# Kernel tuning notes

Hardware: AMD Instinct MI355X
Metric: run time of the kernel (lower is better)

Reference implementation:

```python
import jax, jax.numpy as jnp
import numpy as np

N = 200000          # nodes
E = 800000          # edges (avg degree ~4, molecular graphs)
F_IN = 128          # dataset.num_node_features
HID = 32            # hidden_channels -> widths 32, 64, 128
N_TASKS = 128       # dataset.num_tasks
G = 8000            # number of graphs in the batch
EPS = 1e-5


def _glorot(key, shape):
    fan_in, fan_out = shape[0], shape[1]
    lim = np.sqrt(6.0 / (fan_in + fan_out)).astype(np.float32)
    return jax.random.uniform(key, shape, jnp.float32, -lim, lim)


def setup_inputs() -> dict:
    key = jax.random.key(0)
    ks = jax.random.split(key, 16)
    x = jax.random.normal(ks[0], (N, F_IN), jnp.float32)
    edge_index = jax.random.randint(ks[1], (2, E), 0, N, jnp.int64)
    batch = jnp.sort(jax.random.randint(ks[2], (N,), 0, G, jnp.int64))
    return {
        "x": x,
        "edge_index": edge_index,
        "batch": batch,
        "norm_w": jnp.ones((1,), jnp.float32),
        "norm_b": jnp.zeros((1,), jnp.float32),
        "W1": _glorot(ks[3], (F_IN, HID)),
        "b1": jnp.zeros((HID,), jnp.float32),
        "W2": _glorot(ks[4], (HID, 2 * HID)),
        "b2": jnp.zeros((2 * HID,), jnp.float32),
        "W3": _glorot(ks[5], (2 * HID, 4 * HID)),
        "b3": jnp.zeros((4 * HID,), jnp.float32),
        "lin1_W": _glorot(ks[6], (4 * HID, 256)),
        "lin1_b": jnp.zeros((256,), jnp.float32),
        "lin2_W": _glorot(ks[7], (256, N_TASKS)),
        "lin2_b": jnp.zeros((N_TASKS,), jnp.float32),
    }


def _instance_norm(x, batch, w, b):
    # PyG InstanceNorm: per-graph, per-channel mean / biased var, scalar affine.
    ones = jnp.ones((x.shape[0], 1), x.dtype)
    cnt = jnp.maximum(jax.ops.segment_sum(ones, batch, num_segments=G), 1.0)  # [G,1]
    mean = jax.ops.segment_sum(x, batch, num_segments=G) / cnt               # [G,C]
    var = jax.ops.segment_sum(x * x, batch, num_segments=G) / cnt - mean * mean
    xn = (x - mean[batch]) * jax.lax.rsqrt(var[batch] + EPS)
    return xn * w + b


def _gcn_conv(x, src, dst, dis, W, b):
    # GCNConv: h = xW; out_i = sum_j (d_i d_j)^{-1/2} h_j over A+I edges; + bias.
    h = x @ W
    msg = h[src] * (dis[src] * dis[dst])[:, None]          # [E, C] gather
    agg = jax.ops.segment_sum(msg, dst, num_segments=x.shape[0])
    agg = agg + h * (dis * dis)[:, None]                   # self-loop term
    return agg + b


def reference(x, edge_index, batch, norm_w, norm_b, W1, b1, W2, b2, W3, b3,
              lin1_W, lin1_b, lin2_W, lin2_b):
    src, dst = edge_index[0], edge_index[1]
    # degrees on A + I (all edge weights 1)
    deg = 1.0 + jax.ops.segment_sum(jnp.ones((E,), x.dtype), dst, num_segments=N)
    dis = jax.lax.rsqrt(deg)                                # deg >= 1, safe

    h = _instance_norm(x, batch, norm_w, norm_b)
    h = jax.nn.relu(_gcn_conv(h, src, dst, dis, W1, b1))
    h = jax.nn.relu(_gcn_conv(h, src, dst, dis, W2, b2))
    h = jax.nn.relu(_gcn_conv(h, src, dst, dis, W3, b3))

    # global_max_pool; empty graphs -> 0 (values are >=0 post-relu)
    pooled = jnp.maximum(jax.ops.segment_max(h, batch, num_segments=G), 0.0)

    out = jax.nn.relu(pooled @ lin1_W + lin1_b)
    return out @ lin2_W + lin2_b
```

## Files before the change

### kernel.cpp

```cpp
#include <hip/hip_runtime.h>
#include <hip/hip_bf16.h>
#include <stdint.h>

#define NN 200000
#define NE 800000
#define FIN 128
#define NG 8000
#define EPSV 1e-5f
#define NBS ((NN + 255) / 256)

static __device__ __forceinline__ void u2f(uint4 v, float4& lo, float4& hi) {
    lo.x = __uint_as_float(v.x << 16); lo.y = __uint_as_float(v.x & 0xffff0000u);
    lo.z = __uint_as_float(v.y << 16); lo.w = __uint_as_float(v.y & 0xffff0000u);
    hi.x = __uint_as_float(v.z << 16); hi.y = __uint_as_float(v.z & 0xffff0000u);
    hi.z = __uint_as_float(v.w << 16); hi.w = __uint_as_float(v.w & 0xffff0000u);
}
static __device__ __forceinline__ unsigned int pk(float a, float b) {
    __hip_bfloat16 x = __float2bfloat16(a), y = __float2bfloat16(b);
    return (unsigned int)(*(unsigned short*)&x) | ((unsigned int)(*(unsigned short*)&y) << 16);
}

__global__ void k_cnt(const int* __restrict__ dst, int* __restrict__ cnt) {
    int e = blockIdx.x * 256 + threadIdx.x;
    if (e < NE) atomicAdd(&cnt[dst[e]], 1);
}

__global__ void k_blocksum(const int* __restrict__ cnt, int* __restrict__ bsum) {
    __shared__ int sh[256];
    int b = blockIdx.x, t = threadIdx.x;
    int idx = b * 256 + t;
    sh[t] = (idx < NN) ? cnt[idx] : 0;
    __syncthreads();
    for (int o = 128; o > 0; o >>= 1) {
        if (t < o) sh[t] += sh[t + o];
        __syncthreads();
    }
    if (t == 0) bsum[b] = sh[0];
}

__global__ __launch_bounds__(1024) void k_scanb(const int* __restrict__ bsum, int* __restrict__ bpre) {
    __shared__ int sh[1024];
    int t = threadIdx.x;
    int v = (t < NBS) ? bsum[t] : 0;
    sh[t] = v;
    __syncthreads();
    for (int o = 1; o < 1024; o <<= 1) {
        int add = (t >= o) ? sh[t - o] : 0;
        __syncthreads();
        sh[t] += add;
        __syncthreads();
    }
    if (t < NBS) bpre[t] = sh[t] - v;
}

__global__ void k_scanchunk(const int* __restrict__ cnt, const int* __restrict__ bpre,
                            int* __restrict__ rowstart) {
    __shared__ int sh[256];
    int b = blockIdx.x, t = threadIdx.x;
    int idx = b * 256 + t;
    int v = (idx < NN) ? cnt[idx] : 0;
    sh[t] = v;
    __syncthreads();
    for (int o = 1; o < 256; o <<= 1) {
        int add = (t >= o) ? sh[t - o] : 0;
        __syncthreads();
        sh[t] += add;
        __syncthreads();
    }
    if (idx < NN) rowstart[idx] = bpre[b] + sh[t] - v;
    if (idx == 0) rowstart[NN] = NE;
}

__global__ void k_dis(int* __restrict__ cnt) {
    int n = blockIdx.x * 256 + threadIdx.x;
    if (n < NN) {
        float d = rsqrtf(1.0f + (float)cnt[n]);
        ((float*)cnt)[n] = d;
    }
}

__global__ void k_fill(const int* __restrict__ src, const int* __restrict__ dst,
                       int* __restrict__ cursor, int* __restrict__ csr) {
    int e = blockIdx.x * 256 + threadIdx.x;
    if (e < NE) {
        int pos = atomicAdd(&cursor[dst[e]], 1);
        csr[pos] = src[e];
    }
}

__global__ void k_starts(const int* __restrict__ batch, int* __restrict__ startg) {
    int n = blockIdx.x * 256 + threadIdx.x;
    if (n >= NN) return;
    int b = batch[n];
    int prev = (n == 0) ? -1 : batch[n - 1];
    for (int g = prev + 1; g <= b; ++g) startg[g] = n;
    if (n == NN - 1) {
        for (int g = b + 1; g <= NG; ++g) startg[g] = NN;
    }
}

__global__ __launch_bounds__(256) void k_stats2(const float* __restrict__ x,
                                                const int* __restrict__ startg,
                                                const float* __restrict__ nw,
                                                const float* __restrict__ nb,
                                                float* __restrict__ scale,
                                                float* __restrict__ shift) {
    __shared__ float4 rsum[256], rsq[256];
    int g = blockIdx.x;
    int s = startg[g], e = startg[g + 1];
    if (s == e) return;
    int t = threadIdx.x;
    int slot = t >> 5, c4 = t & 31;
    const float4* x4 = (const float4*)x;
    float4 sum = {0.f, 0.f, 0.f, 0.f}, sq = {0.f, 0.f, 0.f, 0.f};
    for (int n = s + slot; n < e; n += 8) {
        float4 v = x4[n * 32 + c4];
        sum.x += v.x; sum.y += v.y; sum.z += v.z; sum.w += v.w;
        sq.x += v.x * v.x; sq.y += v.y * v.y; sq.z += v.z * v.z; sq.w += v.w * v.w;
    }
    rsum[slot * 32 + c4] = sum;
    rsq[slot * 32 + c4] = sq;
    __syncthreads();
    if (t < 32) {
        float4 S = rsum[t], Q = rsq[t];
#pragma unroll
        for (int sl = 1; sl < 8; ++sl) {
            float4 a = rsum[sl * 32 + t], b = rsq[sl * 32 + t];
            S.x += a.x; S.y += a.y; S.z += a.z; S.w += a.w;
            Q.x += b.x; Q.y += b.y; Q.z += b.z; Q.w += b.w;
        }
        float inv = 1.0f / (float)(e - s);
        float w = nw[0], b = nb[0];
        float4 sc, sh;
        {
            float m = S.x * inv, v = fmaxf(Q.x * inv - m * m, 0.f);
            float is = rsqrtf(v + EPSV); sc.x = is * w; sh.x = b - m * is * w;
        }
        {
            float m = S.y * inv, v = fmaxf(Q.y * inv - m * m, 0.f);
            float is = rsqrtf(v + EPSV); sc.y = is * w; sh.y = b - m * is * w;
        }
        {
            float m = S.z * inv, v = fmaxf(Q.z * inv - m * m, 0.f);
            float is = rsqrtf(v + EPSV); sc.z = is * w; sh.z = b - m * is * w;
        }
        {
            float m = S.w * inv, v = fmaxf(Q.w * inv - m * m, 0.f);
            float is = rsqrtf(v + EPSV); sc.w = is * w; sh.w = b - m * is * w;
        }
        ((float4*)scale)[g * 32 + t] = sc;
        ((float4*)shift)[g * 32 + t] = sh;
    }
}

__global__ __launch_bounds__(256) void k_conv1s(const float* __restrict__ x,
                                                const int* __restrict__ batch,
                                                const float* __restrict__ scale,
                                                const float* __restrict__ shift,
                                                const float* __restrict__ W1,
                                                const float* __restrict__ dis,
                                                float* __restrict__ p1) {
    __shared__ float4 sx4[64 * 33];
    int t = threadIdx.x;
    int base = blockIdx.x * 64;
    const float4* x4 = (const float4*)x;
    const float4* sc4 = (const float4*)scale;
    const float4* sh4 = (const float4*)shift;
    for (int i = t; i < 64 * 32; i += 256) {
        int nl = i >> 5, c4 = i & 31;
        int n = base + nl;
        int g = batch[n];
        float4 xv = x4[n * 32 + c4];
        float4 sc = sc4[g * 32 + c4];
        float4 sh = sh4[g * 32 + c4];
        float4 r;
        r.x = fmaf(xv.x, sc.x, sh.x);
        r.y = fmaf(xv.y, sc.y, sh.y);
        r.z = fmaf(xv.z, sc.z, sh.z);
        r.w = fmaf(xv.w, sc.w, sh.w);
        sx4[nl * 33 + c4] = r;
    }
    __syncthreads();
    int lane = t & 63;
    int kq = __builtin_amdgcn_readfirstlane(t >> 6) * 2;
    const float4* W4 = (const float4*)W1;
    const float4* arow = &sx4[lane * 33];
    float4 acc0 = {0.f, 0.f, 0.f, 0.f}, acc1 = {0.f, 0.f, 0.f, 0.f};
#pragma unroll 4
    for (int c4 = 0; c4 < 32; ++c4) {
        float4 a = arow[c4];
        int rb = c4 * 32 + kq;
        float4 wA0 = W4[rb +  0], wA1 = W4[rb +  1];
        float4 wB0 = W4[rb +  8], wB1 = W4[rb +  9];
        float4 wC0 = W4[rb + 16], wC1 = W4[rb + 17];
        float4 wD0 = W4[rb + 24], wD1 = W4[rb + 25];
        acc0.x += a.x * wA0.x + a.y * wB0.x + a.z * wC0.x + a.w * wD0.x;
        acc0.y += a.x * wA0.y + a.y * wB0.y + a.z * wC0.y + a.w * wD0.y;
        acc0.z += a.x * wA0.z + a.y * wB0.z + a.z * wC0.z + a.w * wD0.z;
        acc0.w += a.x * wA0.w + a.y * wB0.w + a.z * wC0.w + a.w * wD0.w;
        acc1.x += a.x * wA1.x + a.y * wB1.x + a.z * wC1.x + a.w * wD1.x;
        acc1.y += a.x * wA1.y + a.y * wB1.y + a.z * wC1.y + a.w * wD1.y;
        acc1.z += a.x * wA1.z + a.y * wB1.z + a.z * wC1.z + a.w * wD1.z;
        acc1.w += a.x * wA1.w + a.y * wB1.w + a.z * wC1.w + a.w * wD1.w;
    }
    int n = base + lane;
    float d = dis[n];
    float4 r0, r1;
    r0.x = acc0.x * d; r0.y = acc0.y * d; r0.z = acc0.z * d; r0.w = acc0.w * d;
    r1.x = acc1.x * d; r1.y = acc1.y * d; r1.z = acc1.z * d; r1.w = acc1.w * d;
    ((float4*)p1)[n * 8 + kq] = r0;
    ((float4*)p1)[n * 8 + kq + 1] = r1;
}

__global__ __launch_bounds__(256) void k_gather1(const float* __restrict__ p1,
                                                 const int* __restrict__ rowstart,
                                                 const int* __restrict__ csr,
                                                 const float* __restrict__ dis,
                                                 const float* __restrict__ b1,
                                                 float* __restrict__ p2) {
    int tid = blockIdx.x * 256 + threadIdx.x;
    int n = tid >> 3, c4 = tid & 7;
    const float4* p1_4 = (const float4*)p1;
    int s = rowstart[n], e = rowstart[n + 1];
    float4 agg = p1_4[n * 8 + c4];
    int j = s;
    for (; j + 1 < e; j += 2) {
        float4 v0 = p1_4[csr[j] * 8 + c4];
        float4 v1 = p1_4[csr[j + 1] * 8 + c4];
        agg.x += v0.x + v1.x; agg.y += v0.y + v1.y;
        agg.z += v0.z + v1.z; agg.w += v0.w + v1.w;
    }
    if (j < e) {
        float4 v = p1_4[csr[j] * 8 + c4];
        agg.x += v.x; agg.y += v.y; agg.z += v.z; agg.w += v.w;
    }
    float d = dis[n];
    float4 bb = ((const float4*)b1)[c4];
    float4 r;
    r.x = fmaxf(d * agg.x + bb.x, 0.f) * d;
    r.y = fmaxf(d * agg.y + bb.y, 0.f) * d;
    r.z = fmaxf(d * agg.z + bb.z, 0.f) * d;
    r.w = fmaxf(d * agg.w + bb.w, 0.f) * d;
    ((float4*)p2)[n * 8 + c4] = r;
}

__global__ __launch_bounds__(256) void k_conv2g(const float* __restrict__ p2,
                                                const int* __restrict__ rowstart,
                                                const int* __restrict__ csr,
                                                const float* __restrict__ dis,
                                                const float* __restrict__ W2,
                                                const float* __restrict__ b2v,
                                                __hip_bfloat16* __restrict__ p3h) {
    __shared__ float sW[32 * 64];
    __shared__ float4 spart[16 * 16];
    __shared__ float sa[16 * 32];
    int t = threadIdx.x;
    const float4* W4 = (const float4*)W2;
    for (int i = t; i < 32 * 64 / 4; i += 256) ((float4*)sW)[i] = W4[i];
    int base = blockIdx.x * 16;
    const float4* p2_4 = (const float4*)p2;
    {
        int node = t >> 4, c4 = t & 7, half = (t >> 3) & 1;
        int n = base + node;
        int s = rowstart[n], e = rowstart[n + 1];
        float4 agg = {0.f, 0.f, 0.f, 0.f};
        if (half == 0) {
            agg = p2_4[n * 8 + c4];
            for (int j = s; j < e; j += 2) {
                float4 v = p2_4[csr[j] * 8 + c4];
                agg.x += v.x; agg.y += v.y; agg.z += v.z; agg.w += v.w;
            }
        } else {
            for (int j = s + 1; j < e; j += 2) {
                float4 v = p2_4[csr[j] * 8 + c4];
                agg.x += v.x; agg.y += v.y; agg.z += v.z; agg.w += v.w;
            }
        }
        spart[node * 16 + half * 8 + c4] = agg;
    }
    __syncthreads();
    if (t < 128) {
        int nd = t >> 3, cc = t & 7;
        float4 a = spart[nd * 16 + cc], b = spart[nd * 16 + 8 + cc];
        float d = dis[base + nd];
        float4 r;
        r.x = d * (a.x + b.x); r.y = d * (a.y + b.y);
        r.z = d * (a.z + b.z); r.w = d * (a.w + b.w);
        ((float4*)sa)[nd * 8 + cc] = r;
    }
    __syncthreads();
    int k = t & 63, grp = t >> 6;
    float acc[4] = {0.f, 0.f, 0.f, 0.f};
    for (int c = 0; c < 32; ++c) {
        float w = sW[c * 64 + k];
#pragma unroll
        for (int q = 0; q < 4; ++q) acc[q] += sa[(grp * 4 + q) * 32 + c] * w;
    }
    float bb = b2v[k];
#pragma unroll
    for (int q = 0; q < 4; ++q) {
        int n = base + grp * 4 + q;
        float h = fmaxf(acc[q] + bb, 0.f);
        p3h[n * 64 + k] = __float2bfloat16(h * dis[n]);
    }
}

__global__ __launch_bounds__(256) void k_gather3(const __hip_bfloat16* __restrict__ p3h,
                                                 const int* __restrict__ rowstart,
                                                 const int* __restrict__ csr,
                                                 const float* __restrict__ dis,
                                                 __hip_bfloat16* __restrict__ a3h) {
    int tid = blockIdx.x * 256 + threadIdx.x;
    int n = tid >> 3, c8 = tid & 7;
    const uint4* p3q = (const uint4*)p3h;
    int s = rowstart[n], e = rowstart[n + 1];
    float4 alo, ahi;
    u2f(p3q[n * 8 + c8], alo, ahi);
    int j = s;
    for (; j + 1 < e; j += 2) {
        float4 l0, h0, l1, h1;
        u2f(p3q[csr[j] * 8 + c8], l0, h0);
        u2f(p3q[csr[j + 1] * 8 + c8], l1, h1);
        alo.x += l0.x + l1.x; alo.y += l0.y + l1.y;
        alo.z += l0.z + l1.z; alo.w += l0.w + l1.w;
        ahi.x += h0.x + h1.x; ahi.y += h0.y + h1.y;
        ahi.z += h0.z + h1.z; ahi.w += h0.w + h1.w;
    }
    if (j < e) {
        float4 l0, h0;
        u2f(p3q[csr[j] * 8 + c8], l0, h0);
        alo.x += l0.x; alo.y += l0.y; alo.z += l0.z; alo.w += l0.w;
        ahi.x += h0.x; ahi.y += h0.y; ahi.z += h0.z; ahi.w += h0.w;
    }
    float d = dis[n];
    uint4 o;
    o.x = pk(d * alo.x, d * alo.y);
    o.y = pk(d * alo.z, d * alo.w);
    o.z = pk(d * ahi.x, d * ahi.y);
    o.w = pk(d * ahi.z, d * ahi.w);
    ((uint4*)a3h)[n * 8 + c8] = o;
}

__global__ __launch_bounds__(256) void k_conv3s(const __hip_bfloat16* __restrict__ a3h,
                                                const float* __restrict__ W3,
                                                const float* __restrict__ b3v,
                                                const int* __restrict__ batch,
                                                unsigned int* __restrict__ pooled) {
    __shared__ uint4 sa[64 * 9];
    __shared__ float sp[64 * 132];
    __shared__ int sbatch[64];
    int t = threadIdx.x;
    int base = blockIdx.x * 64;
    if (t < 64) sbatch[t] = batch[base + t];
    const uint4* a3q = (const uint4*)a3h;
    for (int i = t; i < 64 * 8; i += 256) {
        sa[(i >> 3) * 9 + (i & 7)] = a3q[(size_t)base * 8 + i];
    }
    __syncthreads();
    int lane = t & 63;
    int kq = __builtin_amdgcn_readfirstlane(t >> 6) * 8;
    const float4* W4 = (const float4*)W3;
    const uint4* arow = &sa[lane * 9];
    float4 acc[8];
#pragma unroll
    for (int j = 0; j < 8; ++j) acc[j] = {0.f, 0.f, 0.f, 0.f};
#pragma unroll 2
    for (int q = 0; q < 8; ++q) {
        float4 lo, hi;
        u2f(arow[q], lo, hi);
        float av[8] = {lo.x, lo.y, lo.z, lo.w, hi.x, hi.y, hi.z, hi.w};
#pragma unroll
        for (int r = 0; r < 8; ++r) {
            float ar = av[r];
            int rb = (q * 8 + r) * 32 + kq;
#pragma unroll
            for (int j = 0; j < 8; ++j) {
                float4 wv = W4[rb + j];
                acc[j].x += ar * wv.x;
                acc[j].y += ar * wv.y;
                acc[j].z += ar * wv.z;
                acc[j].w += ar * wv.w;
            }
        }
    }
    const float4* B4 = (const float4*)b3v;
    float* sprow = &sp[lane * 132];
#pragma unroll
    for (int j = 0; j < 8; ++j) {
        float4 bb = B4[kq + j];
        float4 h;
        h.x = fmaxf(acc[j].x + bb.x, 0.f);
        h.y = fmaxf(acc[j].y + bb.y, 0.f);
        h.z = fmaxf(acc[j].z + bb.z, 0.f);
        h.w = fmaxf(acc[j].w + bb.w, 0.f);
        *(float4*)&sprow[(kq + j) * 4] = h;
    }
    __syncthreads();
    int k4 = t & 31, n0 = (t >> 5) * 8;
    int curg = sbatch[n0];
    float4 cm = {0.f, 0.f, 0.f, 0.f};
#pragma unroll
    for (int ii = 0; ii < 8; ++ii) {
        int g = sbatch[n0 + ii];
        float4 h = *(const float4*)&sp[(n0 + ii) * 132 + k4 * 4];
        if (g != curg) {
            atomicMax(&pooled[curg * 128 + k4 * 4 + 0], __float_as_uint(cm.x));
            atomicMax(&pooled[curg * 128 + k4 * 4 + 1], __float_as_uint(cm.y));
            atomicMax(&pooled[curg * 128 + k4 * 4 + 2], __float_as_uint(cm.z));
            atomicMax(&pooled[curg * 128 + k4 * 4 + 3], __float_as_uint(cm.w));
            cm = {0.f, 0.f, 0.f, 0.f};
            curg = g;
        }
        cm.x = fmaxf(cm.x, h.x);
        cm.y = fmaxf(cm.y, h.y);
        cm.z = fmaxf(cm.z, h.z);
        cm.w = fmaxf(cm.w, h.w);
    }
    atomicMax(&pooled[curg * 128 + k4 * 4 + 0], __float_as_uint(cm.x));
    atomicMax(&pooled[curg * 128 + k4 * 4 + 1], __float_as_uint(cm.y));
    atomicMax(&pooled[curg * 128 + k4 * 4 + 2], __float_as_uint(cm.z));
    atomicMax(&pooled[curg * 128 + k4 * 4 + 3], __float_as_uint(cm.w));
}

__global__ __launch_bounds__(256) void k_lin1(const float* __restrict__ pooled,
                                              const float* __restrict__ W,
                                              const float* __restrict__ bias,
                                              float* __restrict__ mid) {
    __shared__ float sp[8 * 128];
    int t = threadIdx.x;
    int base = blockIdx.x * 8;
    for (int i = t; i < 8 * 128; i += 256) sp[i] = pooled[base * 128 + i];
    __syncthreads();
    float acc[8] = {0.f, 0.f, 0.f, 0.f, 0.f, 0.f, 0.f, 0.f};
    for (int c = 0; c < 128; ++c) {
        float w = W[c * 256 + t];
#pragma unroll
        for (int gl = 0; gl < 8; ++gl) acc[gl] += sp[gl * 128 + c] * w;
    }
    float bb = bias[t];
#pragma unroll
    for (int gl = 0; gl < 8; ++gl) mid[(base + gl) * 256 + t] = fmaxf(acc[gl] + bb, 0.f);
}

__global__ __launch_bounds__(128) void k_lin2(const float* __restrict__ mid,
                                              const float* __restrict__ W,
                                              const float* __restrict__ bias,
                                              float* __restrict__ out) {
    __shared__ float sm[16 * 256];
    int t = threadIdx.x;
    int base = blockIdx.x * 16;
    for (int i = t; i < 16 * 256; i += 128) sm[i] = mid[base * 256 + i];
    __syncthreads();
    float acc[16];
#pragma unroll
    for (int i = 0; i < 16; ++i) acc[i] = 0.f;
    for (int c = 0; c < 256; ++c) {
        float w = W[c * 128 + t];
#pragma unroll
        for (int gl = 0; gl < 16; ++gl) acc[gl] += sm[gl * 256 + c] * w;
    }
    float bb = bias[t];
#pragma unroll
    for (int gl = 0; gl < 16; ++gl)
        out[(base + gl) * 128 + t] = acc[gl] + bb;
}

extern "C" void kernel_launch(void* const* d_in, const int* in_sizes, int n_in,
                              void* d_out, int out_size, void* d_ws, size_t ws_size,
                              hipStream_t stream) {
    (void)in_sizes; (void)n_in; (void)out_size; (void)ws_size;
    const float* x   = (const float*)d_in[0];
    const int* ei    = (const int*)d_in[1];
    const int* src = ei;
    const int* dst = ei + NE;
    const int* batch = (const int*)d_in[2];
    const float* nw  = (const float*)d_in[3];
    const float* nb  = (const float*)d_in[4];
    const float* W1  = (const float*)d_in[5];
    const float* b1  = (const float*)d_in[6];
    const float* W2  = (const float*)d_in[7];
    const float* b2  = (const float*)d_in[8];
    const float* W3  = (const float*)d_in[9];
    const float* b3  = (const float*)d_in[10];
    const float* l1W = (const float*)d_in[11];
    const float* l1b = (const float*)d_in[12];
    const float* l2W = (const float*)d_in[13];
    const float* l2b = (const float*)d_in[14];
    float* out = (float*)d_out;

    char* wsp = (char*)d_ws;
    int*   cnt      = (int*)wsp;   wsp += (size_t)NN * 4;
    int*   rowstart = (int*)wsp;   wsp += (size_t)(NN + 1) * 4;
    int*   cursor   = (int*)wsp;   wsp += (size_t)NN * 4;
    int*   bsum     = (int*)wsp;   wsp += (size_t)NBS * 4;
    int*   bpre     = (int*)wsp;   wsp += (size_t)NBS * 4;
    int*   startg   = (int*)wsp;   wsp += (size_t)(NG + 1) * 4;
    int*   csr      = (int*)wsp;   wsp += (size_t)NE * 4;
    wsp += ((256 - ((uintptr_t)wsp & 255)) & 255);
    float* scale   = (float*)wsp; wsp += (size_t)NG * 128 * 4;
    float* shift   = (float*)wsp; wsp += (size_t)NG * 128 * 4;
    float* pooled  = (float*)wsp; wsp += (size_t)NG * 128 * 4;
    float* regionA = (float*)wsp; wsp += (size_t)NN * 64 * 4;
    float* regionB = (float*)wsp; wsp += (size_t)NN * 64 * 4;

    float* dis  = (float*)cnt;
    float* p1   = regionA;
    float* p2   = regionA + (size_t)NN * 32;
    __hip_bfloat16* p3h = (__hip_bfloat16*)regionB;
    __hip_bfloat16* a3h = (__hip_bfloat16*)regionA;
    float* mid  = regionB;

    hipMemsetAsync(cnt, 0, (size_t)NN * 4, stream);
    k_cnt<<<(NE + 255) / 256, 256, 0, stream>>>(dst, cnt);
    k_blocksum<<<NBS, 256, 0, stream>>>(cnt, bsum);
    k_scanb<<<1, 1024, 0, stream>>>(bsum, bpre);
    k_scanchunk<<<NBS, 256, 0, stream>>>(cnt, bpre, rowstart);
    k_dis<<<(NN + 255) / 256, 256, 0, stream>>>(cnt);
    hipMemcpyAsync(cursor, rowstart, (size_t)NN * 4, hipMemcpyDeviceToDevice, stream);
    k_fill<<<(NE + 255) / 256, 256, 0, stream>>>(src, dst, cursor, csr);

    k_starts<<<(NN + 255) / 256, 256, 0, stream>>>(batch, startg);
    k_stats2<<<NG, 256, 0, stream>>>(x, startg, nw, nb, scale, shift);
    k_conv1s<<<NN / 64, 256, 0, stream>>>(x, batch, scale, shift, W1, dis, p1);
    k_gather1<<<NN * 8 / 256, 256, 0, stream>>>(p1, rowstart, csr, dis, b1, p2);
    k_conv2g<<<NN / 16, 256, 0, stream>>>(p2, rowstart, csr, dis, W2, b2, p3h);
    k_gather3<<<NN * 8 / 256, 256, 0, stream>>>(p3h, rowstart, csr, dis, a3h);
    hipMemsetAsync(pooled, 0, (size_t)NG * 128 * 4, stream);
    k_conv3s<<<NN / 64, 256, 0, stream>>>(a3h, W3, b3, batch, (unsigned int*)pooled);

    k_lin1<<<NG / 8, 256, 0, stream>>>(pooled, l1W, l1b, mid);
    k_lin2<<<NG / 16, 128, 0, stream>>>(mid, l2W, l2b, out);
}
```

Measured before the change: 558.0 us.

## Use bf16 MFMA with hi/lo split weights for conv3 GEMM

Replaces the scalar FP32 FMA loop in the third GCN layer's dense transform with MFMA 16x16x32 bf16 instructions. W3 is split once per call into bf16 high and low parts so the product keeps near-FP32 weight precision, at the cost of two MFMAs per tile. The aim is to cut VALU work and global weight loads in k_conv3. It adds a small preprocessing kernel and new workspace buffers.

```diff
diff --git a/kernel.cpp b/kernel.cpp
--- a/kernel.cpp
+++ b/kernel.cpp
@@ -8,6 +8,13 @@
 #define NG 8000
 #define EPSV 1e-5f
 #define NBS ((NN + 255) / 256)
+
+typedef __attribute__((ext_vector_type(8))) short bf16x8;
+typedef __attribute__((ext_vector_type(4))) float f32x4;
+
+static __device__ __forceinline__ bf16x8 as_bf16x8(uint4 u) {
+    union { uint4 u; bf16x8 v; } c; c.u = u; return c.v;
+}
 
 static __device__ __forceinline__ void u2f(uint4 v, float4& lo, float4& hi) {
     lo.x = __uint_as_float(v.x << 16); lo.y = __uint_as_float(v.x & 0xffff0000u);
@@ -97,6 +104,20 @@
     if (n == NN - 1) {
         for (int g = b + 1; g <= NG; ++g) startg[g] = NN;
     }
+}
+
+__global__ __launch_bounds__(256) void k_w3split(const float* __restrict__ W3,
+                                                 unsigned short* __restrict__ whi,
+                                                 unsigned short* __restrict__ wlo) {
+    int i = blockIdx.x * 256 + threadIdx.x;
+    if (i >= 64 * 128) return;
+    int n = i >> 6, k = i & 63;
+    float w = W3[k * 128 + n];
+    __hip_bfloat16 h = __float2bfloat16(w);
+    float hf = __bfloat162float(h);
+    __hip_bfloat16 l = __float2bfloat16(w - hf);
+    whi[n * 64 + k] = *(unsigned short*)&h;
+    wlo[n * 64 + k] = *(unsigned short*)&l;
 }
 
 __global__ __launch_bounds__(256) void k_stats2(const float* __restrict__ x,
@@ -341,8 +362,9 @@
     ((uint4*)a3h)[n * 8 + c8] = o;
 }
 
-__global__ __launch_bounds__(256) void k_conv3s(const __hip_bfloat16* __restrict__ a3h,
-                                                const float* __restrict__ W3,
+__global__ __launch_bounds__(256) void k_conv3m(const __hip_bfloat16* __restrict__ a3h,
+                                                const unsigned short* __restrict__ w3hi,
+                                                const unsigned short* __restrict__ w3lo,
                                                 const float* __restrict__ b3v,
                                                 const int* __restrict__ batch,
                                                 unsigned int* __restrict__ pooled) {
@@ -357,43 +379,51 @@
         sa[(i >> 3) * 9 + (i & 7)] = a3q[(size_t)base * 8 + i];
     }
     __syncthreads();
-    int lane = t & 63;
-    int kq = __builtin_amdgcn_readfirstlane(t >> 6) * 8;
-    const float4* W4 = (const float4*)W3;
-    const uint4* arow = &sa[lane * 9];
-    float4 acc[8];
-#pragma unroll
-    for (int j = 0; j < 8; ++j) acc[j] = {0.f, 0.f, 0.f, 0.f};
-#pragma unroll 2
-    for (int q = 0; q < 8; ++q) {
-        float4 lo, hi;
-        u2f(arow[q], lo, hi);
-        float av[8] = {lo.x, lo.y, lo.z, lo.w, hi.x, hi.y, hi.z, hi.w};
-#pragma unroll
-        for (int r = 0; r < 8; ++r) {
-            float ar = av[r];
-            int rb = (q * 8 + r) * 32 + kq;
-#pragma unroll
-            for (int j = 0; j < 8; ++j) {
-                float4 wv = W4[rb + j];
-                acc[j].x += ar * wv.x;
-                acc[j].y += ar * wv.y;
-                acc[j].z += ar * wv.z;
-                acc[j].w += ar * wv.w;
+    int lane = t & 63, w = t >> 6;
+    int h = lane >> 4;
+    int cid = lane & 15;
+    const uint4* WHq = (const uint4*)w3hi;
+    const uint4* WLq = (const uint4*)w3lo;
+    uint4 bh[2][2], bl[2][2];
+#pragma unroll
+    for (int nl = 0; nl < 2; ++nl) {
+        int n = (w * 2 + nl) * 16 + cid;
+#pragma unroll
+        for (int kt = 0; kt < 2; ++kt) {
+            bh[nl][kt] = WHq[n * 8 + kt * 4 + h];
+            bl[nl][kt] = WLq[n * 8 + kt * 4 + h];
+        }
+    }
+    f32x4 acc[2][4];
+#pragma unroll
+    for (int nl = 0; nl < 2; ++nl)
+#pragma unroll
+        for (int mi = 0; mi < 4; ++mi) acc[nl][mi] = {0.f, 0.f, 0.f, 0.f};
+#pragma unroll
+    for (int mi = 0; mi < 4; ++mi) {
+        int arow = (mi * 16 + cid) * 9;
+        bf16x8 a0 = as_bf16x8(sa[arow + h]);
+        bf16x8 a1 = as_bf16x8(sa[arow + 4 + h]);
+#pragma unroll
+        for (int nl = 0; nl < 2; ++nl) {
+            acc[nl][mi] = __builtin_amdgcn_mfma_f32_16x16x32_bf16(a0, as_bf16x8(bh[nl][0]), acc[nl][mi], 0, 0, 0);
+            acc[nl][mi] = __builtin_amdgcn_mfma_f32_16x16x32_bf16(a1, as_bf16x8(bh[nl][1]), acc[nl][mi], 0, 0, 0);
+            acc[nl][mi] = __builtin_amdgcn_mfma_f32_16x16x32_bf16(a0, as_bf16x8(bl[nl][0]), acc[nl][mi], 0, 0, 0);
+            acc[nl][mi] = __builtin_amdgcn_mfma_f32_16x16x32_bf16(a1, as_bf16x8(bl[nl][1]), acc[nl][mi], 0, 0, 0);
+        }
+    }
+#pragma unroll
+    for (int nl = 0; nl < 2; ++nl) {
+        int ch = (w * 2 + nl) * 16 + cid;
+        float bb = b3v[ch];
+#pragma unroll
+        for (int mi = 0; mi < 4; ++mi) {
+#pragma unroll
+            for (int r = 0; r < 4; ++r) {
+                int node_l = mi * 16 + h * 4 + r;
+                sp[node_l * 132 + ch] = fmaxf(acc[nl][mi][r] + bb, 0.f);
             }
         }
-    }
-    const float4* B4 = (const float4*)b3v;
-    float* sprow = &sp[lane * 132];
-#pragma unroll
-    for (int j = 0; j < 8; ++j) {
-        float4 bb = B4[kq + j];
-        float4 h;
-        h.x = fmaxf(acc[j].x + bb.x, 0.f);
-        h.y = fmaxf(acc[j].y + bb.y, 0.f);
-        h.z = fmaxf(acc[j].z + bb.z, 0.f);
-        h.w = fmaxf(acc[j].w + bb.w, 0.f);
-        *(float4*)&sprow[(kq + j) * 4] = h;
     }
     __syncthreads();
     int k4 = t & 31, n0 = (t >> 5) * 8;
@@ -402,7 +432,7 @@
 #pragma unroll
     for (int ii = 0; ii < 8; ++ii) {
         int g = sbatch[n0 + ii];
-        float4 h = *(const float4*)&sp[(n0 + ii) * 132 + k4 * 4];
+        float4 hv = *(const float4*)&sp[(n0 + ii) * 132 + k4 * 4];
         if (g != curg) {
             atomicMax(&pooled[curg * 128 + k4 * 4 + 0], __float_as_uint(cm.x));
             atomicMax(&pooled[curg * 128 + k4 * 4 + 1], __float_as_uint(cm.y));
@@ -411,10 +441,10 @@
             cm = {0.f, 0.f, 0.f, 0.f};
             curg = g;
         }
-        cm.x = fmaxf(cm.x, h.x);
-        cm.y = fmaxf(cm.y, h.y);
-        cm.z = fmaxf(cm.z, h.z);
-        cm.w = fmaxf(cm.w, h.w);
+        cm.x = fmaxf(cm.x, hv.x);
+        cm.y = fmaxf(cm.y, hv.y);
+        cm.z = fmaxf(cm.z, hv.z);
+        cm.w = fmaxf(cm.w, hv.w);
     }
     atomicMax(&pooled[curg * 128 + k4 * 4 + 0], __float_as_uint(cm.x));
     atomicMax(&pooled[curg * 128 + k4 * 4 + 1], __float_as_uint(cm.y));
@@ -497,6 +527,8 @@
     int*   startg   = (int*)wsp;   wsp += (size_t)(NG + 1) * 4;
     int*   csr      = (int*)wsp;   wsp += (size_t)NE * 4;
     wsp += ((256 - ((uintptr_t)wsp & 255)) & 255);
+    unsigned short* w3hi = (unsigned short*)wsp; wsp += (size_t)128 * 64 * 2;
+    unsigned short* w3lo = (unsigned short*)wsp; wsp += (size_t)128 * 64 * 2;
     float* scale   = (float*)wsp; wsp += (size_t)NG * 128 * 4;
     float* shift   = (float*)wsp; wsp += (size_t)NG * 128 * 4;
     float* pooled  = (float*)wsp; wsp += (size_t)NG * 128 * 4;
@@ -518,6 +550,7 @@
     k_dis<<<(NN + 255) / 256, 256, 0, stream>>>(cnt);
     hipMemcpyAsync(cursor, rowstart, (size_t)NN * 4, hipMemcpyDeviceToDevice, stream);
     k_fill<<<(NE + 255) / 256, 256, 0, stream>>>(src, dst, cursor, csr);
+    k_w3split<<<32, 256, 0, stream>>>(W3, w3hi, w3lo);
 
     k_starts<<<(NN + 255) / 256, 256, 0, stream>>>(batch, startg);
     k_stats2<<<NG, 256, 0, stream>>>(x, startg, nw, nb, scale, shift);
@@ -526,7 +559,7 @@
     k_conv2g<<<NN / 16, 256, 0, stream>>>(p2, rowstart, csr, dis, W2, b2, p3h);
     k_gather3<<<NN * 8 / 256, 256, 0, stream>>>(p3h, rowstart, csr, dis, a3h);
     hipMemsetAsync(pooled, 0, (size_t)NG * 128 * 4, stream);
-    k_conv3s<<<NN / 64, 256, 0, stream>>>(a3h, W3, b3, batch, (unsigned int*)pooled);
+    k_conv3m<<<NN / 64, 256, 0, stream>>>(a3h, w3hi, w3lo, b3, batch, (unsigned int*)pooled);
 
     k_lin1<<<NG / 8, 256, 0, stream>>>(pooled, l1W, l1b, mid);
     k_lin2<<<NG / 16, 128, 0, stream>>>(mid, l2W, l2b, out);
```

Measured after the change: 532.0 us. 1.05x faster.
